# Kernel tuning notes

Hardware: AMD Instinct MI355X
Metric: run time of the kernel (lower is better)

Reference implementation:

```python
import jax, jax.numpy as jnp
import numpy as np
from jax import lax

IN_DIM, OUT_DIM, GROUPS, K, DEGREE, PAD = 64, 128, 4, 3, 3, 1
IN_G = IN_DIM // GROUPS    # 16
OUT_G = OUT_DIM // GROUPS  # 32
EPS = 1e-5


def setup_inputs() -> dict:
    key = jax.random.key(0)
    k1, k2 = jax.random.split(key)
    x = jax.random.normal(k1, (64, IN_DIM, 64, 64), jnp.float32)
    # meta (hypernetwork-generated) weight: (out_g, in_g*(degree+2), k, k)
    layer_weight = jax.random.normal(k2, (OUT_G, IN_G * (DEGREE + 2), K, K), jnp.float32) * 0.05
    return {"x": x, "layer_weight": layer_weight}


def _conv(x, w):
    # plain NCHW conv2d, groups=1, stride=1, dilation=1, symmetric padding
    return lax.conv_general_dilated(
        x, w, window_strides=(1, 1), padding=[(PAD, PAD), (PAD, PAD)],
        dimension_numbers=("NCHW", "OIHW", "NCHW"))


def _legendre_basis(x, order):
    # recursive Legendre polynomials P0..P_order, concatenated on channel dim
    polys = [jnp.ones_like(x), x]
    for n in range(1, order):
        pn = ((2.0 * n + 1.0) * x * polys[-1] - n * polys[-2]) / (n + 1.0)
        polys.append(pn)
    return jnp.concatenate(polys, axis=1)  # [B, in_g*(order+1), H, W]


def _group_forward(xg, w):
    # xg: [B, in_g, H, W]; w: [out_g, in_g*(degree+2), k, k]
    base_w = w[:, :IN_G]                                   # (out_g, in_g, k, k)
    base_out = _conv(jax.nn.silu(xg), base_w)
    # global min-max normalization over the whole group tensor
    xmin, xmax = xg.min(), xg.max()
    x_norm = 2.0 * (xg - xmin) / (xmax - xmin) - 1.0
    lb = _legendre_basis(x_norm, DEGREE)                   # [B, in_g*(degree+1), H, W]
    poly_w = w[:, IN_G:].reshape(OUT_G, IN_G * (DEGREE + 1), K, K)
    y = base_out + _conv(lb, poly_w)
    # InstanceNorm2d (affine=False, no running stats): per-sample per-channel
    mean = y.mean(axis=(2, 3), keepdims=True)
    var = y.var(axis=(2, 3), keepdims=True)
    y = (y - mean) * lax.rsqrt(var + EPS)
    return jax.nn.silu(y)


def reference(x, layer_weight):
    B, C, H, W = x.shape
    # split channels into groups, vmap over groups (same weight for each group)
    xg = x.reshape(B, GROUPS, IN_G, H, W).transpose(1, 0, 2, 3, 4)  # [G,B,in_g,H,W]
    yg = jax.vmap(lambda xx: _group_forward(xx, layer_weight))(xg)  # [G,B,out_g,H,W]
    return yg.transpose(1, 0, 2, 3, 4).reshape(B, OUT_DIM, H, W)
```

## Files before the change

kernel.cpp:

```cpp
#include <hip/hip_runtime.h>
#include <hip/hip_bf16.h>


#define NB 64
#define NH 64
#define NW 64

typedef __attribute__((ext_vector_type(8)))  short bf16x8;
typedef __attribute__((ext_vector_type(8)))  unsigned short u16x8;
typedef __attribute__((ext_vector_type(16))) float f32x16;

__device__ __forceinline__ float silu(float v) {
    return v / (1.0f + __expf(-v));
}
__device__ __forceinline__ unsigned short tobf(float f) {
    union { __hip_bfloat16 h; unsigned short u; } cv;
    cv.h = __float2bfloat16(f);
    return cv.u;
}

__global__ __launch_bounds__(256) void minmax_kernel(const float* __restrict__ x,
                                                     float* __restrict__ pmm) {
    int plane = blockIdx.x;
    const float4* p = (const float4*)(x + (size_t)plane * 4096);
    int t = threadIdx.x;
    float mn = 3.4e38f, mx = -3.4e38f;
    #pragma unroll
    for (int k = 0; k < 4; ++k) {
        float4 v = p[t + k * 256];
        mn = fminf(mn, fminf(fminf(v.x, v.y), fminf(v.z, v.w)));
        mx = fmaxf(mx, fmaxf(fmaxf(v.x, v.y), fmaxf(v.z, v.w)));
    }
    #pragma unroll
    for (int off = 32; off; off >>= 1) {
        mn = fminf(mn, __shfl_xor(mn, off));
        mx = fmaxf(mx, __shfl_xor(mx, off));
    }
    __shared__ float smn[4], smx[4];
    int wid = t >> 6, lane = t & 63;
    if (lane == 0) { smn[wid] = mn; smx[wid] = mx; }
    __syncthreads();
    if (t == 0) {
        mn = fminf(fminf(smn[0], smn[1]), fminf(smn[2], smn[3]));
        mx = fmaxf(fmaxf(smx[0], smx[1]), fmaxf(smx[2], smx[3]));
        pmm[plane * 2]     = mn;
        pmm[plane * 2 + 1] = mx;
    }
}

__global__ __launch_bounds__(256) void reduce_repack_kernel(const float* __restrict__ pmm,
                                                            const float* __restrict__ w,
                                                            float* __restrict__ wsf,
                                                            unsigned short* __restrict__ wpk,
                                                            float* __restrict__ Tt) {
    int blk = blockIdx.x;
    int t = threadIdx.x;
    if (blk < 4) {
        int g = blk;
        float mn = 3.4e38f, mx = -3.4e38f;
        #pragma unroll
        for (int j = 0; j < 4; ++j) {
            int p = t + j * 256;
            int b = p >> 4, c = p & 15;
            int plane = b * 64 + g * 16 + c;
            mn = fminf(mn, pmm[plane * 2]);
            mx = fmaxf(mx, pmm[plane * 2 + 1]);
        }
        #pragma unroll
        for (int off = 32; off; off >>= 1) {
            mn = fminf(mn, __shfl_xor(mn, off));
            mx = fmaxf(mx, __shfl_xor(mx, off));
        }
        __shared__ float smn[4], smx[4];
        int wid = t >> 6, lane = t & 63;
        if (lane == 0) { smn[wid] = mn; smx[wid] = mx; }
        __syncthreads();
        if (t == 0) {
            mn = fminf(fminf(smn[0], smn[1]), fminf(smn[2], smn[3]));
            mx = fmaxf(fmaxf(smx[0], smx[1]), fmaxf(smx[2], smx[3]));
            wsf[g * 2]     = mn;
            wsf[g * 2 + 1] = mx;
        }
    } else if (blk < 76) {
        int idx = (blk - 4) * 256 + t;
        int p   = idx / 4608;
        int r1  = idx - p * 4608;
        int tap = r1 / 512;
        int r2  = r1 - tap * 512;
        int h   = r2 >> 8;
        int oc  = (r2 >> 3) & 31;
        int j   = r2 & 7;
        int k   = p * 16 + h * 8 + j;
        int orig = (k < 16) ? k : (k + 16);
        wpk[idx] = tobf(w[oc * 720 + orig * 9 + tap]);
    } else {
        for (int i = t; i < 288; i += 256) {
            int oc = i / 9, ty = i - oc * 9;
            int ey = ty / 3, ex = ty - ey * 3;
            int ky0 = (ey == 0) ? 1 : 0, ky1 = (ey == 2) ? 1 : 2;
            int kx0 = (ex == 0) ? 1 : 0, kx1 = (ex == 2) ? 1 : 2;
            float s = 0.f;
            for (int c = 0; c < 16; ++c)
                for (int ky = ky0; ky <= ky1; ++ky)
                    for (int kx = kx0; kx <= kx1; ++kx)
                        s += w[oc * 720 + (16 + c) * 9 + ky * 3 + kx];
            Tt[i] = s;
        }
    }
}

__global__ __launch_bounds__(512, 4) void conv_mfma_kernel(const float* __restrict__ x,
                                                           const float* __restrict__ wsf,
                                                           const unsigned short* __restrict__ wpk,
                                                           const float* __restrict__ Tt,
                                                           float* __restrict__ out,
                                                           unsigned short* __restrict__ yscr) {
    __shared__ unsigned short wl[18432];
    __shared__ unsigned short aug2[2][5184];
    __shared__ float Tl[288];

    int flat = blockIdx.x;
    int f = ((flat & 7) << 9) | (flat >> 3);
    int tile = f & 15;
    int bg = f >> 4;
    int b = bg & 63;
    int g = bg >> 6;
    int th0 = (tile >> 2) * 16, tw0 = (tile & 3) * 16;

    float xmin = wsf[g * 2];
    float xmax = wsf[g * 2 + 1];
    float inv = 2.0f / (xmax - xmin);

    const float* xg = x + ((size_t)b * 64 + g * 16) * 4096;
    int t = threadIdx.x;

    {
        const uint4* srcw = (const uint4*)wpk;
        uint4* dstw = (uint4*)wl;
        #pragma unroll
        for (int i = 0; i < 5; ++i) {
            int idx = t + i * 512;
            if (idx < 2304) dstw[idx] = srcw[idx];
        }
    }
    if (t < 288) Tl[t] = Tt[t];

    float r[2][8];
    bool okv[2];
    #pragma unroll
    for (int i = 0; i < 2; ++i) {
        okv[i] = false;
        int idx = t + i * 512;
        if (idx < 648) {
            int half = idx >= 324 ? 1 : 0;
            int pix = idx - half * 324;
            int ly = pix / 18, lx = pix - ly * 18;
            int gh = th0 + ly - 1, gw = tw0 + lx - 1;
            bool ok = (gh >= 0 && gh < NH && gw >= 0 && gw < NW);
            okv[i] = ok;
            const float* s = xg + (size_t)(half * 8) * 4096 + gh * 64 + gw;
            #pragma unroll
            for (int j = 0; j < 8; ++j)
                r[i][j] = ok ? s[(size_t)j * 4096] : 0.f;
        }
    }

    int wv = t >> 6;
    int lane = t & 63;
    int lo = lane & 31, hi = lane >> 5;
    int py = 2 * wv + (lo >> 4), px = lo & 15;

    auto stage = [&](int p, unsigned short* buf) {
        #pragma unroll
        for (int i = 0; i < 2; ++i) {
            int idx = t + i * 512;
            if (idx < 648) {
                int half = idx >= 324 ? 1 : 0;
                int pix = idx - half * 324;
                bf16x8 v;
                #pragma unroll
                for (int j = 0; j < 8; ++j) {
                    float val = r[i][j];
                    float o;
                    if (p == 0) {
                        o = silu(val);
                    } else {
                        float xn = (val - xmin) * inv - 1.f;
                        if (p == 1) o = xn;
                        else {
                            float x2 = xn * xn;
                            o = (p == 2) ? (1.5f * x2 - 0.5f)
                                         : ((2.5f * x2 - 1.5f) * xn);
                        }
                        o = okv[i] ? o : 0.f;
                    }
                    v[j] = (short)tobf(o);
                }
                *(bf16x8*)&buf[(half * 324 + pix) * 8] = v;
            }
        }
    };

    stage(0, aug2[0]);
    __syncthreads();

    f32x16 acc = {};

    #pragma unroll
    for (int p = 0; p < 4; ++p) {
        const int cb = p & 1, nb = cb ^ 1;

        if (p < 3) stage(p + 1, aug2[nb]);

        #pragma unroll
        for (int tap = 0; tap < 9; ++tap) {
            const int ky = tap / 3, kx = tap % 3;
            const int hp = (py + ky) * 18 + (px + kx);
            bf16x8 Af = *(const bf16x8*)&wl[(((p * 9 + tap) * 2 + hi) * 32 + lo) * 8];
            bf16x8 Bf = *(const bf16x8*)&aug2[cb][(hi * 324 + hp) * 8];
            acc = __builtin_amdgcn_mfma_f32_32x32x16_bf16(Af, Bf, acc, 0, 0, 0);
        }

        __syncthreads();
    }

    int h = th0 + py, wc = tw0 + px;
    int ey = (h == 0) ? 0 : ((h == NH - 1) ? 2 : 1);
    int ex = (wc == 0) ? 0 : ((wc == NW - 1) ? 2 : 1);
    int et = ey * 3 + ex;
    size_t obase = ((size_t)b * 128 + g * 32) * 4096 + (size_t)h * 64 + wc;
    if (yscr) {
        #pragma unroll
        for (int rr = 0; rr < 16; ++rr) {
            int oc = (rr & 3) + 8 * (rr >> 2) + 4 * hi;
            yscr[obase + (size_t)oc * 4096] = tobf(acc[rr] + Tl[oc * 9 + et]);
        }
    } else {
        #pragma unroll
        for (int rr = 0; rr < 16; ++rr) {
            int oc = (rr & 3) + 8 * (rr >> 2) + 4 * hi;
            out[obase + (size_t)oc * 4096] = acc[rr] + Tl[oc * 9 + et];
        }
    }
}

__global__ __launch_bounds__(256) void norm_bf16_kernel(const unsigned short* __restrict__ yscr,
                                                        float* __restrict__ out) {
    int plane = blockIdx.x;
    const u16x8* p = (const u16x8*)(yscr + (size_t)plane * 4096);
    int t = threadIdx.x;
    float v[2][8];
    float s = 0.f, s2 = 0.f;
    #pragma unroll
    for (int k = 0; k < 2; ++k) {
        u16x8 u = p[t + k * 256];
        #pragma unroll
        for (int j = 0; j < 8; ++j) {
            float f = __uint_as_float((unsigned)u[j] << 16);
            v[k][j] = f;
            s += f;
            s2 += f * f;
        }
    }
    #pragma unroll
    for (int off = 32; off; off >>= 1) {
        s  += __shfl_xor(s, off);
        s2 += __shfl_xor(s2, off);
    }
    __shared__ float ss[4], ss2[4];
    int wid = t >> 6, lane = t & 63;
    if (lane == 0) { ss[wid] = s; ss2[wid] = s2; }
    __syncthreads();
    s  = ss[0] + ss[1] + ss[2] + ss[3];
    s2 = ss2[0] + ss2[1] + ss2[2] + ss2[3];
    float mean = s * (1.f / 4096.f);
    float var  = fmaxf(s2 * (1.f / 4096.f) - mean * mean, 0.f);
    float istd = rsqrtf(var + 1e-5f);
    float4* o = (float4*)(out + (size_t)plane * 4096);
    #pragma unroll
    for (int k = 0; k < 2; ++k) {
        float4 a, bq;
        a.x = silu((v[k][0] - mean) * istd);
        a.y = silu((v[k][1] - mean) * istd);
        a.z = silu((v[k][2] - mean) * istd);
        a.w = silu((v[k][3] - mean) * istd);
        bq.x = silu((v[k][4] - mean) * istd);
        bq.y = silu((v[k][5] - mean) * istd);
        bq.z = silu((v[k][6] - mean) * istd);
        bq.w = silu((v[k][7] - mean) * istd);
        o[(t + k * 256) * 2]     = a;
        o[(t + k * 256) * 2 + 1] = bq;
    }
}

__global__ __launch_bounds__(256) void norm_kernel(float* __restrict__ out) {
    int plane = blockIdx.x;
    float4* p = (float4*)(out + (size_t)plane * 4096);
    int t = threadIdx.x;
    float4 v[4];
    float s = 0.f, s2 = 0.f;
    #pragma unroll
    for (int k = 0; k < 4; ++k) {
        v[k] = p[t + k * 256];
        s  += v[k].x + v[k].y + v[k].z + v[k].w;
        s2 += v[k].x * v[k].x + v[k].y * v[k].y + v[k].z * v[k].z + v[k].w * v[k].w;
    }
    #pragma unroll
    for (int off = 32; off; off >>= 1) {
        s  += __shfl_xor(s, off);
        s2 += __shfl_xor(s2, off);
    }
    __shared__ float ss[4], ss2[4];
    int wid = t >> 6, lane = t & 63;
    if (lane == 0) { ss[wid] = s; ss2[wid] = s2; }
    __syncthreads();
    s  = ss[0] + ss[1] + ss[2] + ss[3];
    s2 = ss2[0] + ss2[1] + ss2[2] + ss2[3];
    float mean = s * (1.f / 4096.f);
    float var  = fmaxf(s2 * (1.f / 4096.f) - mean * mean, 0.f);
    float istd = rsqrtf(var + 1e-5f);
    #pragma unroll
    for (int k = 0; k < 4; ++k) {
        float4 o;
        o.x = (v[k].x - mean) * istd; o.x = silu(o.x);
        o.y = (v[k].y - mean) * istd; o.y = silu(o.y);
        o.z = (v[k].z - mean) * istd; o.z = silu(o.z);
        o.w = (v[k].w - mean) * istd; o.w = silu(o.w);
        p[t + k * 256] = o;
    }
}

extern "C" void kernel_launch(void* const* d_in, const int* in_sizes, int n_in,
                              void* d_out, int out_size, void* d_ws, size_t ws_size,
                              hipStream_t stream) {
    const float* x = (const float*)d_in[0];
    const float* w = (const float*)d_in[1];
    float* out = (float*)d_out;
    float* wsf = (float*)d_ws;
    float* pmm = (float*)((char*)d_ws + 64);
    unsigned short* wpk = (unsigned short*)((char*)d_ws + 64 + 32768);
    float* Tt = (float*)((char*)d_ws + 64 + 32768 + 36864);

    const size_t YSCR_OFF = 131072;
    const size_t YSCR_BYTES = (size_t)64 * 128 * 4096 * 2;
    unsigned short* yscr = (ws_size >= YSCR_OFF + YSCR_BYTES)
                         ? (unsigned short*)((char*)d_ws + YSCR_OFF) : nullptr;

    hipLaunchKernelGGL(minmax_kernel, dim3(NB * 64), dim3(256), 0, stream, x, pmm);
    hipLaunchKernelGGL(reduce_repack_kernel, dim3(77), dim3(256), 0, stream, pmm, w, wsf, wpk, Tt);
    hipLaunchKernelGGL(conv_mfma_kernel, dim3(4096), dim3(512), 0, stream, x, wsf, wpk, Tt, out, yscr);
    if (yscr)
        hipLaunchKernelGGL(norm_bf16_kernel, dim3(NB * 128), dim3(256), 0, stream, yscr, out);
    else
        hipLaunchKernelGGL(norm_kernel, dim3(NB * 128), dim3(256), 0, stream, out);
}
```

Before: 137.0 us.

## Widen conv tile to 16x32 with two accumulators, single-buffer staging

Each block now computes a 16x32 output tile instead of 16x16, issuing two MFMAs per weight fragment load so the A operand and the per-block weight LDS copy are reused across twice as many pixels. The grid halves to 2048 blocks. The double-buffered input staging is replaced with a single buffer and an extra barrier per polynomial stage, so staging no longer overlaps with MFMA work. The change also raises register use (three rows of prefetched inputs, two accumulators), which may reduce occupancy.

New measurement: 129.4 us. -5.5%, faster.

```diff
diff --git a/kernel.cpp b/kernel.cpp
--- a/kernel.cpp
+++ b/kernel.cpp
@@ -116,16 +116,16 @@
                                                            float* __restrict__ out,
                                                            unsigned short* __restrict__ yscr) {
     __shared__ unsigned short wl[18432];
-    __shared__ unsigned short aug2[2][5184];
+    __shared__ unsigned short augp[9792];
     __shared__ float Tl[288];
 
     int flat = blockIdx.x;
-    int f = ((flat & 7) << 9) | (flat >> 3);
-    int tile = f & 15;
-    int bg = f >> 4;
+    int f = ((flat & 7) << 8) | (flat >> 3);
+    int q = f & 7;
+    int bg = f >> 3;
     int b = bg & 63;
     int g = bg >> 6;
-    int th0 = (tile >> 2) * 16, tw0 = (tile & 3) * 16;
+    int th0 = (q >> 1) * 16, tw0 = (q & 1) * 32;
 
     float xmin = wsf[g * 2];
     float xmax = wsf[g * 2 + 1];
@@ -145,16 +145,16 @@
     }
     if (t < 288) Tl[t] = Tt[t];
 
-    float r[2][8];
-    bool okv[2];
-    #pragma unroll
-    for (int i = 0; i < 2; ++i) {
+    float r[3][8];
+    bool okv[3];
+    #pragma unroll
+    for (int i = 0; i < 3; ++i) {
         okv[i] = false;
         int idx = t + i * 512;
-        if (idx < 648) {
-            int half = idx >= 324 ? 1 : 0;
-            int pix = idx - half * 324;
-            int ly = pix / 18, lx = pix - ly * 18;
+        if (idx < 1224) {
+            int half = idx >= 612 ? 1 : 0;
+            int pix = idx - half * 612;
+            int ly = pix / 34, lx = pix - ly * 34;
             int gh = th0 + ly - 1, gw = tw0 + lx - 1;
             bool ok = (gh >= 0 && gh < NH && gw >= 0 && gw < NW);
             okv[i] = ok;
@@ -170,13 +170,16 @@
     int lo = lane & 31, hi = lane >> 5;
     int py = 2 * wv + (lo >> 4), px = lo & 15;
 
-    auto stage = [&](int p, unsigned short* buf) {
-        #pragma unroll
-        for (int i = 0; i < 2; ++i) {
+    f32x16 acc0 = {}, acc1 = {};
+
+    #pragma unroll
+    for (int p = 0; p < 4; ++p) {
+        #pragma unroll
+        for (int i = 0; i < 3; ++i) {
             int idx = t + i * 512;
-            if (idx < 648) {
-                int half = idx >= 324 ? 1 : 0;
-                int pix = idx - half * 324;
+            if (idx < 1224) {
+                int half = idx >= 612 ? 1 : 0;
+                int pix = idx - half * 612;
                 bf16x8 v;
                 #pragma unroll
                 for (int j = 0; j < 8; ++j) {
@@ -196,50 +199,50 @@
                     }
                     v[j] = (short)tobf(o);
                 }
-                *(bf16x8*)&buf[(half * 324 + pix) * 8] = v;
+                *(bf16x8*)&augp[(half * 612 + pix) * 8] = v;
             }
         }
-    };
-
-    stage(0, aug2[0]);
-    __syncthreads();
-
-    f32x16 acc = {};
-
-    #pragma unroll
-    for (int p = 0; p < 4; ++p) {
-        const int cb = p & 1, nb = cb ^ 1;
-
-        if (p < 3) stage(p + 1, aug2[nb]);
+        __syncthreads();
 
         #pragma unroll
         for (int tap = 0; tap < 9; ++tap) {
             const int ky = tap / 3, kx = tap % 3;
-            const int hp = (py + ky) * 18 + (px + kx);
+            const int hp = (py + ky) * 34 + (px + kx);
             bf16x8 Af = *(const bf16x8*)&wl[(((p * 9 + tap) * 2 + hi) * 32 + lo) * 8];
-            bf16x8 Bf = *(const bf16x8*)&aug2[cb][(hi * 324 + hp) * 8];
-            acc = __builtin_amdgcn_mfma_f32_32x32x16_bf16(Af, Bf, acc, 0, 0, 0);
-        }
-
+            bf16x8 Bf0 = *(const bf16x8*)&augp[(hi * 612 + hp) * 8];
+            bf16x8 Bf1 = *(const bf16x8*)&augp[(hi * 612 + hp + 16) * 8];
+            acc0 = __builtin_amdgcn_mfma_f32_32x32x16_bf16(Af, Bf0, acc0, 0, 0, 0);
+            acc1 = __builtin_amdgcn_mfma_f32_32x32x16_bf16(Af, Bf1, acc1, 0, 0, 0);
+        }
         __syncthreads();
     }
 
-    int h = th0 + py, wc = tw0 + px;
+    int h = th0 + py;
     int ey = (h == 0) ? 0 : ((h == NH - 1) ? 2 : 1);
-    int ex = (wc == 0) ? 0 : ((wc == NW - 1) ? 2 : 1);
-    int et = ey * 3 + ex;
-    size_t obase = ((size_t)b * 128 + g * 32) * 4096 + (size_t)h * 64 + wc;
+    size_t gbase = ((size_t)b * 128 + g * 32) * 4096 + (size_t)h * 64;
+
+    int wc0 = tw0 + px;
+    int ex0 = (wc0 == 0) ? 0 : ((wc0 == NW - 1) ? 2 : 1);
+    int et0 = ey * 3 + ex0;
+    int wc1 = tw0 + 16 + px;
+    int ex1 = (wc1 == 0) ? 0 : ((wc1 == NW - 1) ? 2 : 1);
+    int et1 = ey * 3 + ex1;
+
     if (yscr) {
         #pragma unroll
         for (int rr = 0; rr < 16; ++rr) {
             int oc = (rr & 3) + 8 * (rr >> 2) + 4 * hi;
-            yscr[obase + (size_t)oc * 4096] = tobf(acc[rr] + Tl[oc * 9 + et]);
+            size_t o = gbase + (size_t)oc * 4096;
+            yscr[o + wc0] = tobf(acc0[rr] + Tl[oc * 9 + et0]);
+            yscr[o + wc1] = tobf(acc1[rr] + Tl[oc * 9 + et1]);
         }
     } else {
         #pragma unroll
         for (int rr = 0; rr < 16; ++rr) {
             int oc = (rr & 3) + 8 * (rr >> 2) + 4 * hi;
-            out[obase + (size_t)oc * 4096] = acc[rr] + Tl[oc * 9 + et];
+            size_t o = gbase + (size_t)oc * 4096;
+            out[o + wc0] = acc0[rr] + Tl[oc * 9 + et0];
+            out[o + wc1] = acc1[rr] + Tl[oc * 9 + et1];
         }
     }
 }
@@ -348,7 +351,7 @@
 
     hipLaunchKernelGGL(minmax_kernel, dim3(NB * 64), dim3(256), 0, stream, x, pmm);
     hipLaunchKernelGGL(reduce_repack_kernel, dim3(77), dim3(256), 0, stream, pmm, w, wsf, wpk, Tt);
-    hipLaunchKernelGGL(conv_mfma_kernel, dim3(4096), dim3(512), 0, stream, x, wsf, wpk, Tt, out, yscr);
+    hipLaunchKernelGGL(conv_mfma_kernel, dim3(2048), dim3(512), 0, stream, x, wsf, wpk, Tt, out, yscr);
     if (yscr)
         hipLaunchKernelGGL(norm_bf16_kernel, dim3(NB * 128), dim3(256), 0, stream, yscr, out);
     else
```
